# Kernel tuning notes

Hardware: AMD Instinct MI355X
Metric: run time of the kernel (lower is better)

Reference implementation:

```python
import jax, jax.numpy as jnp
import numpy as np

N, E, D_IN, HID, HEADS, D_OUT, R = 20000, 640000, 256, 128, 4, 128, 32
NEG_SLOPE = 0.2  # PyG GATConv default


def setup_inputs() -> dict:
    key = jax.random.key(0)
    ks = jax.random.split(key, 12)
    s = 0.05
    return {
        "x": jax.random.normal(ks[0], (N, D_IN), jnp.float32),
        "edge_index": jax.random.randint(ks[1], (2, E), 0, N, dtype=jnp.int64),
        "edge_type": jax.random.randint(ks[2], (E,), 0, R, dtype=jnp.int64),
        "rel_emb": jax.random.normal(ks[3], (R, D_IN), jnp.float32) * s,
        "W1": jax.random.normal(ks[4], (D_IN, HEADS * HID), jnp.float32) * s,
        "att_src1": jax.random.normal(ks[5], (HEADS, HID), jnp.float32) * s,
        "att_dst1": jax.random.normal(ks[6], (HEADS, HID), jnp.float32) * s,
        "b1": jnp.zeros((HEADS * HID,), jnp.float32),
        "W2": jax.random.normal(ks[7], (HEADS * HID, D_OUT), jnp.float32) * s,
        "att_src2": jax.random.normal(ks[8], (1, D_OUT), jnp.float32) * s,
        "att_dst2": jax.random.normal(ks[9], (1, D_OUT), jnp.float32) * s,
        "b2": jnp.zeros((D_OUT,), jnp.float32),
    }


def _gat_conv(x, src, dst, W, a_src, a_dst, bias, heads, ch):
    """PyG GATConv (eval mode, self loops already in src/dst)."""
    n = x.shape[0]
    h = (x @ W).reshape(n, heads, ch)                      # [N,H,C]
    alpha_s = jnp.einsum('nhc,hc->nh', h, a_src)           # [N,H]
    alpha_d = jnp.einsum('nhc,hc->nh', h, a_dst)
    e = jax.nn.leaky_relu(alpha_s[src] + alpha_d[dst], NEG_SLOPE)  # [E,H]
    # segment softmax over incoming edges of each dst node
    m = jax.ops.segment_max(e, dst, num_segments=n)        # [N,H]
    p = jnp.exp(e - m[dst])
    denom = jax.ops.segment_sum(p, dst, num_segments=n)
    alpha = p / (denom[dst] + 1e-16)                       # [E,H]
    out = jax.ops.segment_sum(h[src] * alpha[:, :, None], dst, num_segments=n)
    return out.reshape(n, heads * ch) + bias


def reference(x, edge_index, edge_type, rel_emb, W1, att_src1, att_dst1, b1,
              W2, att_src2, att_dst2, b2):
    src, dst = edge_index[0], edge_index[1]
    # relational feature injection: x_mod[src] += rel_emb[edge_type]
    x_mod = x.at[src].add(rel_emb[edge_type])
    # GATConv adds self loops by default
    loop = jnp.arange(N, dtype=src.dtype)
    s2 = jnp.concatenate([src, loop])
    d2 = jnp.concatenate([dst, loop])
    h = _gat_conv(x_mod, s2, d2, W1, att_src1, att_dst1, b1, HEADS, HID)
    h = jax.nn.elu(h)
    return _gat_conv(h, s2, d2, W2, att_src2, att_dst2, b2, 1, D_OUT)
```

## Files before the change

kernel.cpp:

```cpp
#include <hip/hip_runtime.h>


#define D_IN   256
#define HID1   512
#define NHEADS 4
#define CH1    128
#define DOUT   128
#define NREL   32
#define NEG_SLOPE 0.2f
#define M_PAD  20096

static __device__ __forceinline__ float b2f(unsigned short u) {
  union { unsigned int i; float f; } v; v.i = ((unsigned int)u) << 16; return v.f;
}
static __device__ __forceinline__ unsigned short f2b(float f) {
  union { float f; unsigned int i; } v; v.f = f;
  unsigned int x = v.i;
  return (unsigned short)((x + 0x7fffu + ((x >> 16) & 1u)) >> 16);
}
static __device__ __forceinline__ float lrelu(float x) {
  return x > 0.f ? x : NEG_SLOPE * x;
}
static __device__ __forceinline__ void acc8(float* acc, float w, uint4 r) {
  unsigned int u;
  union { unsigned int i; float f; } cl, ch;
  u = r.x; cl.i = u << 16; ch.i = u & 0xffff0000u; acc[0] += w * cl.f; acc[1] += w * ch.f;
  u = r.y; cl.i = u << 16; ch.i = u & 0xffff0000u; acc[2] += w * cl.f; acc[3] += w * ch.f;
  u = r.z; cl.i = u << 16; ch.i = u & 0xffff0000u; acc[4] += w * cl.f; acc[5] += w * ch.f;
  u = r.w; cl.i = u << 16; ch.i = u & 0xffff0000u; acc[6] += w * cl.f; acc[7] += w * ch.f;
}

typedef __attribute__((ext_vector_type(8))) short bf16x8;
typedef __attribute__((ext_vector_type(4))) float f32x4;

__global__ void prep_kernel(const int* __restrict__ src, const int* __restrict__ dst,
                            const int* __restrict__ et, int* __restrict__ counts,
                            int* __restrict__ deg, int E, int eb,
                            const float* __restrict__ W1, const float* __restrict__ W2,
                            unsigned short* __restrict__ W1T, unsigned short* __restrict__ W2T) {
  int b = blockIdx.x;
  if (b < eb) {
    int e = b * 256 + threadIdx.x;
    if (e >= E) return;
    atomicAdd(&counts[(size_t)src[e] * NREL + et[e]], 1);
    atomicAdd(&deg[dst[e]], 1);
  } else {
    int idx = (b - eb) * 256 + threadIdx.x;
    if (idx < D_IN * HID1) {
      int r = idx / HID1, c = idx % HID1;
      W1T[(size_t)c * D_IN + r] = f2b(W1[idx]);
    } else {
      int k = idx - D_IN * HID1;
      if (k < HID1 * DOUT) {
        int r = k / DOUT, c = k % DOUT;
        W2T[(size_t)c * HID1 + r] = f2b(W2[k]);
      }
    }
  }
}

__global__ void scan_local(const int* __restrict__ in, int* __restrict__ out,
                           int* __restrict__ bsum, int n) {
  __shared__ int wsum[4];
  int t = threadIdx.x;
  int base = blockIdx.x * 1024 + t * 4;
  int v0 = (base + 0 < n) ? in[base + 0] : 0;
  int v1 = (base + 1 < n) ? in[base + 1] : 0;
  int v2 = (base + 2 < n) ? in[base + 2] : 0;
  int v3 = (base + 3 < n) ? in[base + 3] : 0;
  int s = v0 + v1 + v2 + v3;
  int lane = t & 63, w = t >> 6;
  int sc = s;
  for (int off = 1; off < 64; off <<= 1) {
    int u = __shfl_up(sc, off);
    if (lane >= off) sc += u;
  }
  if (lane == 63) wsum[w] = sc;
  __syncthreads();
  int woff = 0;
  for (int i = 0; i < w; ++i) woff += wsum[i];
  int excl = woff + sc - s;
  if (base + 0 < n) out[base + 0] = excl;
  if (base + 1 < n) out[base + 1] = excl + v0;
  if (base + 2 < n) out[base + 2] = excl + v0 + v1;
  if (base + 3 < n) out[base + 3] = excl + v0 + v1 + v2;
  if (t == 255) bsum[blockIdx.x] = woff + sc;
}

__global__ void scan_blocks(int* __restrict__ bsum, int nb,
                            int* __restrict__ offsets, int n) {
  int t = threadIdx.x;
  int v = (t < nb) ? bsum[t] : 0;
  int sc = v;
  for (int off = 1; off < 64; off <<= 1) {
    int u = __shfl_up(sc, off);
    if (t >= off) sc += u;
  }
  if (t < nb) bsum[t] = sc - v;
  if (t == nb - 1) offsets[n] = v;
}

__global__ void scatter_kernel(const int* __restrict__ src, const int* __restrict__ dst,
                               const int* __restrict__ offsets, const int* __restrict__ bsum,
                               int* __restrict__ cursor, int* __restrict__ csr_src, int E) {
  int e = blockIdx.x * 256 + threadIdx.x;
  if (e >= E) return;
  int d = dst[e];
  int pos = offsets[d] + bsum[d >> 10] + atomicAdd(&cursor[d], 1);
  csr_src[pos] = src[e];
}

__global__ void xmod_kernel(const float* __restrict__ x,
                            const int* __restrict__ counts,
                            const float* __restrict__ rel,
                            unsigned short* __restrict__ x_modb, int n_nodes) {
  __shared__ int cnt[NREL];
  int node = blockIdx.x;
  if (threadIdx.x < NREL) cnt[threadIdx.x] = counts[(size_t)node * NREL + threadIdx.x];
  __syncthreads();
  int k = threadIdx.x;
  float v = x[(size_t)node * D_IN + k];
  for (int r = 0; r < NREL; ++r) {
    int c = cnt[r];
    if (c) v += (float)c * rel[r * D_IN + k];
  }
  x_modb[(size_t)node * D_IN + k] = f2b(v);
}

template <int BM, int NH>
__global__ __launch_bounds__(256) void mfma_gemm(
    const unsigned short* __restrict__ A, const unsigned short* __restrict__ BT,
    unsigned short* __restrict__ C, int M, int N, int K,
    const float* __restrict__ att_s, const float* __restrict__ att_d,
    float* __restrict__ as_out, float* __restrict__ ad_out) {
  constexpr int MFR = BM / 32;
  __shared__ __align__(16) unsigned short Asl[BM * 32];
  __shared__ __align__(16) unsigned short Bsl[128 * 32];
  int tid = threadIdx.x;
  int m0 = blockIdx.y * BM, n0 = blockIdx.x * 128;
  int lane = tid & 63, wv = tid >> 6;
  int wm = wv & 1, wn = wv >> 1;
  int l16 = lane & 15, quad = lane >> 4;
  int lr = lane >> 2, lseg = lane & 3;

  f32x4 acc[MFR][4];
#pragma unroll
  for (int i = 0; i < MFR; ++i)
#pragma unroll
    for (int j = 0; j < 4; ++j) acc[i][j] = (f32x4)(0.f);

  for (int k0 = 0; k0 < K; k0 += 32) {
#pragma unroll
    for (int c = wv; c < BM / 16; c += 4) {
      int gr = m0 + c * 16 + lr; gr = gr < M ? gr : M - 1;
      __builtin_amdgcn_global_load_lds(
          (const __attribute__((address_space(1))) void*)(A + (size_t)gr * K + k0 + lseg * 8),
          (__attribute__((address_space(3))) void*)(&Asl[c * 512]), 16, 0, 0);
    }
#pragma unroll
    for (int c = wv; c < 8; c += 4) {
      int gr = n0 + c * 16 + lr;
      __builtin_amdgcn_global_load_lds(
          (const __attribute__((address_space(1))) void*)(BT + (size_t)gr * K + k0 + lseg * 8),
          (__attribute__((address_space(3))) void*)(&Bsl[c * 512]), 16, 0, 0);
    }
    __syncthreads();
    bf16x8 af[MFR], bfr[4];
#pragma unroll
    for (int mf = 0; mf < MFR; ++mf)
      af[mf] = *(const bf16x8*)(&Asl[(wm * (BM / 2) + mf * 16 + l16) * 32 + quad * 8]);
#pragma unroll
    for (int nf = 0; nf < 4; ++nf)
      bfr[nf] = *(const bf16x8*)(&Bsl[(wn * 64 + nf * 16 + l16) * 32 + quad * 8]);
#pragma unroll
    for (int mf = 0; mf < MFR; ++mf)
#pragma unroll
      for (int nf = 0; nf < 4; ++nf)
        acc[mf][nf] = __builtin_amdgcn_mfma_f32_16x16x32_bf16(af[mf], bfr[nf], acc[mf][nf], 0, 0, 0);
    __syncthreads();
  }
#pragma unroll
  for (int mf = 0; mf < MFR; ++mf)
#pragma unroll
    for (int nf = 0; nf < 4; ++nf)
#pragma unroll
      for (int r = 0; r < 4; ++r) {
        int row = m0 + wm * (BM / 2) + mf * 16 + quad * 4 + r;
        int col = n0 + wn * 64 + nf * 16 + l16;
        C[(size_t)row * N + col] = f2b(acc[mf][nf][r]);
      }
  int head = blockIdx.x;
  float asw[4], adw[4];
#pragma unroll
  for (int nf = 0; nf < 4; ++nf) {
    int cl = wn * 64 + nf * 16 + l16;
    asw[nf] = att_s[head * 128 + cl];
    adw[nf] = att_d[head * 128 + cl];
  }
#pragma unroll
  for (int mf = 0; mf < MFR; ++mf)
#pragma unroll
    for (int r = 0; r < 4; ++r) {
      float sd = acc[mf][0][r] * asw[0] + acc[mf][1][r] * asw[1] +
                 acc[mf][2][r] * asw[2] + acc[mf][3][r] * asw[3];
      float dd = acc[mf][0][r] * adw[0] + acc[mf][1][r] * adw[1] +
                 acc[mf][2][r] * adw[2] + acc[mf][3][r] * adw[3];
#pragma unroll
      for (int off = 1; off < 16; off <<= 1) {
        sd += __shfl_xor(sd, off);
        dd += __shfl_xor(dd, off);
      }
      int row = m0 + wm * (BM / 2) + mf * 16 + quad * 4 + r;
      if (l16 == 0 && row < M) {
        atomicAdd(&as_out[row * NH + head], sd);
        atomicAdd(&ad_out[row * NH + head], dd);
      }
    }
}

__global__ __launch_bounds__(256) void aggregate1_kernel(
    const unsigned short* __restrict__ h1b,
    const float* __restrict__ as1, const float* __restrict__ ad1,
    const int* __restrict__ offsets, const int* __restrict__ bsum,
    const int* __restrict__ csr_src,
    const float* __restrict__ bias, unsigned short* __restrict__ h2b, int n_nodes) {
  int node = blockIdx.x * 4 + (threadIdx.x >> 6);
  if (node >= n_nodes) return;
  int lane = threadIdx.x & 63;
  int g = lane >> 5, l32 = lane & 31;
  int head = l32 >> 3;
  int lo = offsets[node] + bsum[node >> 10];
  int hi = offsets[node + 1] + bsum[(node + 1) >> 10];
  float4 asn = ((const float4*)as1)[node];
  float4 ad4 = ((const float4*)ad1)[node];
  float ad_own = head == 0 ? ad4.x : head == 1 ? ad4.y : head == 2 ? ad4.z : ad4.w;
  float as_own = head == 0 ? asn.x : head == 1 ? asn.y : head == 2 ? asn.z : asn.w;

  const uint4* h1v = (const uint4*)h1b;
  float acc[16];
#pragma unroll
  for (int k = 0; k < 16; ++k) acc[k] = 0.f;
  float denom = 0.f;

  int nit = (hi - lo + 1) >> 1;
  int j = lo + g;
  bool valid = j < hi;
  int s = valid ? csr_src[j] : node;
  float asv = as1[s * 4 + head];
  for (int i = 0; i < nit; ++i) {
    int jn = j + 2;
    bool vn = jn < hi;
    int sn = vn ? csr_src[jn] : node;
    float asv_n = as1[sn * 4 + head];
    uint4 h0 = h1v[(size_t)s * 64 + l32 * 2];
    uint4 h1r = h1v[(size_t)s * 64 + l32 * 2 + 1];
    float w = valid ? __expf(lrelu(asv + ad_own)) : 0.f;
    acc8(acc, w, h0); acc8(acc + 8, w, h1r);
    denom += w;
    j = jn; valid = vn; s = sn; asv = asv_n;
  }
  if (g == 0) {
    uint4 h0 = h1v[(size_t)node * 64 + l32 * 2];
    uint4 h1r = h1v[(size_t)node * 64 + l32 * 2 + 1];
    float w = __expf(lrelu(as_own + ad_own));
    acc8(acc, w, h0); acc8(acc + 8, w, h1r);
    denom += w;
  }
#pragma unroll
  for (int k = 0; k < 16; ++k) acc[k] += __shfl_xor(acc[k], 32);
  denom += __shfl_xor(denom, 32);
  if (g == 0) {
    float inv = 1.f / (denom + 1e-16f);
    unsigned int od[8];
#pragma unroll
    for (int q = 0; q < 8; ++q) {
      float vlo = acc[2 * q] * inv + bias[l32 * 16 + 2 * q];
      float vhi = acc[2 * q + 1] * inv + bias[l32 * 16 + 2 * q + 1];
      vlo = vlo > 0.f ? vlo : expm1f(vlo);
      vhi = vhi > 0.f ? vhi : expm1f(vhi);
      od[q] = (unsigned int)f2b(vlo) | ((unsigned int)f2b(vhi) << 16);
    }
    uint4 o0; o0.x = od[0]; o0.y = od[1]; o0.z = od[2]; o0.w = od[3];
    uint4 o1; o1.x = od[4]; o1.y = od[5]; o1.z = od[6]; o1.w = od[7];
    ((uint4*)h2b)[(size_t)node * 64 + l32 * 2] = o0;
    ((uint4*)h2b)[(size_t)node * 64 + l32 * 2 + 1] = o1;
  }
}

__global__ __launch_bounds__(256) void aggregate2_kernel(
    const unsigned short* __restrict__ t2b,
    const float* __restrict__ as2, const float* __restrict__ ad2,
    const int* __restrict__ offsets, const int* __restrict__ bsum,
    const int* __restrict__ csr_src,
    const float* __restrict__ bias, float* __restrict__ out, int n_nodes) {
  int node = blockIdx.x * 4 + (threadIdx.x >> 6);
  if (node >= n_nodes) return;
  int lane = threadIdx.x & 63;
  int g = lane >> 4, l16 = lane & 15;
  int lo = offsets[node] + bsum[node >> 10];
  int hi = offsets[node + 1] + bsum[(node + 1) >> 10];
  float ad = ad2[node];

  const uint4* t2v = (const uint4*)t2b;
  float acc[8] = {0.f, 0.f, 0.f, 0.f, 0.f, 0.f, 0.f, 0.f};
  float denom = 0.f;
  int nit = (hi - lo + 3) >> 2;
  int j = lo + g;
  bool valid = j < hi;
  int s = valid ? csr_src[j] : node;
  float asv = as2[s];
  for (int i = 0; i < nit; ++i) {
    int jn = j + 4;
    bool vn = jn < hi;
    int sn = vn ? csr_src[jn] : node;
    float asv_n = as2[sn];
    uint4 tv = t2v[(size_t)s * 16 + l16];
    float w = valid ? __expf(lrelu(asv + ad)) : 0.f;
    acc8(acc, w, tv);
    denom += w;
    j = jn; valid = vn; s = sn; asv = asv_n;
  }
  if (g == 0) {
    uint4 tv = t2v[(size_t)node * 16 + l16];
    float w = __expf(lrelu(as2[node] + ad));
    acc8(acc, w, tv);
    denom += w;
  }
#pragma unroll
  for (int k = 0; k < 8; ++k) {
    acc[k] += __shfl_xor(acc[k], 16);
    acc[k] += __shfl_xor(acc[k], 32);
  }
  denom += __shfl_xor(denom, 16);
  denom += __shfl_xor(denom, 32);
  if (g == 0) {
    float inv = 1.f / (denom + 1e-16f);
    float4 o0, o1;
    o0.x = acc[0] * inv + bias[l16 * 8 + 0];
    o0.y = acc[1] * inv + bias[l16 * 8 + 1];
    o0.z = acc[2] * inv + bias[l16 * 8 + 2];
    o0.w = acc[3] * inv + bias[l16 * 8 + 3];
    o1.x = acc[4] * inv + bias[l16 * 8 + 4];
    o1.y = acc[5] * inv + bias[l16 * 8 + 5];
    o1.z = acc[6] * inv + bias[l16 * 8 + 6];
    o1.w = acc[7] * inv + bias[l16 * 8 + 7];
    *(float4*)(out + (size_t)node * DOUT + l16 * 8) = o0;
    *(float4*)(out + (size_t)node * DOUT + l16 * 8 + 4) = o1;
  }
}

extern "C" void kernel_launch(void* const* d_in, const int* in_sizes, int n_in,
                              void* d_out, int out_size, void* d_ws, size_t ws_size,
                              hipStream_t stream) {
  const float* x     = (const float*)d_in[0];
  const int* ei      = (const int*)d_in[1];
  const int* etype   = (const int*)d_in[2];
  const float* rel   = (const float*)d_in[3];
  const float* W1    = (const float*)d_in[4];
  const float* at_s1 = (const float*)d_in[5];
  const float* at_d1 = (const float*)d_in[6];
  const float* b1    = (const float*)d_in[7];
  const float* W2    = (const float*)d_in[8];
  const float* at_s2 = (const float*)d_in[9];
  const float* at_d2 = (const float*)d_in[10];
  const float* b2v   = (const float*)d_in[11];
  float* out         = (float*)d_out;

  const int N = in_sizes[0] / D_IN;
  const int E = in_sizes[2];
  const int* srcv = ei;
  const int* dstv = ei + E;

  char* p = (char*)d_ws;
  auto carve = [&](size_t bytes) -> char* {
    char* r = p; p += (bytes + 255) & ~(size_t)255; return r;
  };
  int*   counts  = (int*)carve((size_t)N * NREL * 4);
  int*   deg     = (int*)carve((size_t)N * 4);
  int*   offsets = (int*)carve(((size_t)N + 1) * 4);
  int*   cursor  = (int*)carve((size_t)N * 4);
  int*   bsum    = (int*)carve(64 * 4);
  float* as1     = (float*)carve((size_t)N * NHEADS * 4);
  float* ad1     = (float*)carve((size_t)N * NHEADS * 4);
  float* as2     = (float*)carve((size_t)N * 4);
  float* ad2     = (float*)carve((size_t)N * 4);
  size_t zero_bytes = (size_t)(p - (char*)counts);
  int*   csr_src = (int*)carve((size_t)E * 4);
  unsigned short* W1T    = (unsigned short*)carve((size_t)HID1 * D_IN * 2);
  unsigned short* W2T    = (unsigned short*)carve((size_t)DOUT * HID1 * 2);
  unsigned short* x_modb = (unsigned short*)carve((size_t)M_PAD * D_IN * 2);
  unsigned short* h1b    = (unsigned short*)carve((size_t)M_PAD * HID1 * 2);
  unsigned short* h2b    = (unsigned short*)carve((size_t)M_PAD * HID1 * 2);
  unsigned short* t2b    = (unsigned short*)carve((size_t)M_PAD * DOUT * 2);

  hipMemsetAsync(counts, 0, zero_bytes, stream);

  int eb = (E + 255) / 256;
  int cb = (D_IN * HID1 + HID1 * DOUT + 255) / 256;
  int nb = (N + 1023) / 1024;
  prep_kernel<<<eb + cb, 256, 0, stream>>>(srcv, dstv, etype, counts, deg, E, eb,
                                           W1, W2, W1T, W2T);
  scan_local<<<nb, 256, 0, stream>>>(deg, offsets, bsum, N);
  scan_blocks<<<1, 64, 0, stream>>>(bsum, nb, offsets, N);
  scatter_kernel<<<eb, 256, 0, stream>>>(srcv, dstv, offsets, bsum, cursor, csr_src, E);
  xmod_kernel<<<N, 256, 0, stream>>>(x, counts, rel, x_modb, N);
  mfma_gemm<128, NHEADS><<<dim3(HID1 / 128, M_PAD / 128), 256, 0, stream>>>(
      x_modb, W1T, h1b, N, HID1, D_IN, at_s1, at_d1, as1, ad1);
  aggregate1_kernel<<<(N + 3) / 4, 256, 0, stream>>>(h1b, as1, ad1, offsets, bsum,
                                                     csr_src, b1, h2b, N);
  mfma_gemm<64, 1><<<dim3(DOUT / 128, M_PAD / 64), 256, 0, stream>>>(
      h2b, W2T, t2b, N, DOUT, HID1, at_s2, at_d2, as2, ad2);
  aggregate2_kernel<<<(N + 3) / 4, 256, 0, stream>>>(t2b, as2, ad2, offsets, bsum,
                                                     csr_src, b2v, out, N);
}
```

Baseline: 382.0 us.

## Precompute edge weights, stage neighbor rows via LDS loads, fold layer-2 attention into aggregate1

The change adds separate kernels that compute the per-edge softmax numerators (exp of leaky-relu) over the CSR order, which requires building a csr_dst array. The aggregation kernels now gather neighbor feature rows in batches straight into shared memory with global_load_lds, one full wave per node. The layer-2 attention projections are computed algebraically as h2·(W2·att) inside aggregate1, using vectors precomputed in scan_blocks, so the second GEMM no longer needs its atomic alpha epilogue. The xmod kernel is also vectorized to four nodes per block with float4 loads. In exchange it adds two edge-sized kernels, extra workspace traffic for the weights and csr_dst, and explicit waitcnt barriers that serialize each batch's loads.

```diff
diff --git a/kernel.cpp b/kernel.cpp
--- a/kernel.cpp
+++ b/kernel.cpp
@@ -4,15 +4,16 @@
 #define D_IN   256
 #define HID1   512
 #define NHEADS 4
-#define CH1    128
 #define DOUT   128
 #define NREL   32
 #define NEG_SLOPE 0.2f
 #define M_PAD  20096
-
-static __device__ __forceinline__ float b2f(unsigned short u) {
-  union { unsigned int i; float f; } v; v.i = ((unsigned int)u) << 16; return v.f;
-}
+#define DB1    8
+#define DB2    16
+
+#define WAIT_VM0()   __builtin_amdgcn_s_waitcnt(0x0f70)
+#define WAIT_LGKM0() __builtin_amdgcn_s_waitcnt(0xc07f)
+
 static __device__ __forceinline__ unsigned short f2b(float f) {
   union { float f; unsigned int i; } v; v.f = f;
   unsigned int x = v.i;
@@ -88,46 +89,72 @@
 }
 
 __global__ void scan_blocks(int* __restrict__ bsum, int nb,
-                            int* __restrict__ offsets, int n) {
+                            int* __restrict__ offsets, int n,
+                            const float* __restrict__ W2,
+                            const float* __restrict__ att_s2, const float* __restrict__ att_d2,
+                            float* __restrict__ vs, float* __restrict__ vd) {
   int t = threadIdx.x;
-  int v = (t < nb) ? bsum[t] : 0;
-  int sc = v;
-  for (int off = 1; off < 64; off <<= 1) {
-    int u = __shfl_up(sc, off);
-    if (t >= off) sc += u;
-  }
-  if (t < nb) bsum[t] = sc - v;
-  if (t == nb - 1) offsets[n] = v;
+  if (t < 64) {
+    int v = (t < nb) ? bsum[t] : 0;
+    int sc = v;
+    for (int off = 1; off < 64; off <<= 1) {
+      int u = __shfl_up(sc, off);
+      if (t >= off) sc += u;
+    }
+    if (t < nb) bsum[t] = sc - v;
+    if (t == nb - 1) offsets[n] = v;
+  }
+#pragma unroll
+  for (int rr = 0; rr < 2; ++rr) {
+    int r = t * 2 + rr;
+    float ss = 0.f, dd = 0.f;
+    for (int c = 0; c < DOUT; ++c) {
+      float wv = W2[(size_t)r * DOUT + c];
+      ss += wv * att_s2[c];
+      dd += wv * att_d2[c];
+    }
+    vs[r] = ss; vd[r] = dd;
+  }
 }
 
 __global__ void scatter_kernel(const int* __restrict__ src, const int* __restrict__ dst,
                                const int* __restrict__ offsets, const int* __restrict__ bsum,
-                               int* __restrict__ cursor, int* __restrict__ csr_src, int E) {
+                               int* __restrict__ cursor, int* __restrict__ csr_src,
+                               int* __restrict__ csr_dst, int E) {
   int e = blockIdx.x * 256 + threadIdx.x;
   if (e >= E) return;
   int d = dst[e];
   int pos = offsets[d] + bsum[d >> 10] + atomicAdd(&cursor[d], 1);
   csr_src[pos] = src[e];
-}
-
-__global__ void xmod_kernel(const float* __restrict__ x,
-                            const int* __restrict__ counts,
-                            const float* __restrict__ rel,
-                            unsigned short* __restrict__ x_modb, int n_nodes) {
-  __shared__ int cnt[NREL];
-  int node = blockIdx.x;
-  if (threadIdx.x < NREL) cnt[threadIdx.x] = counts[(size_t)node * NREL + threadIdx.x];
-  __syncthreads();
-  int k = threadIdx.x;
-  float v = x[(size_t)node * D_IN + k];
+  csr_dst[pos] = d;
+}
+
+__global__ __launch_bounds__(256) void xmod_kernel(
+    const float* __restrict__ x, const int* __restrict__ counts,
+    const float* __restrict__ rel, unsigned short* __restrict__ x_modb, int n_nodes) {
+  int wv = threadIdx.x >> 6;
+  int node = blockIdx.x * 4 + wv;
+  if (node >= n_nodes) return;
+  int l = threadIdx.x & 63;
+  int cnt_l = counts[(size_t)node * NREL + (l & 31)];
+  const float4* x4 = (const float4*)x;
+  const float4* rel4 = (const float4*)rel;
+  float4 v = x4[(size_t)node * 64 + l];
+#pragma unroll
   for (int r = 0; r < NREL; ++r) {
-    int c = cnt[r];
-    if (c) v += (float)c * rel[r * D_IN + k];
-  }
-  x_modb[(size_t)node * D_IN + k] = f2b(v);
-}
-
-template <int BM, int NH>
+    int c = __shfl(cnt_l, r);
+    if (c) {
+      float4 rv = rel4[r * 64 + l];
+      float fc = (float)c;
+      v.x += fc * rv.x; v.y += fc * rv.y; v.z += fc * rv.z; v.w += fc * rv.w;
+    }
+  }
+  ushort4 o;
+  o.x = f2b(v.x); o.y = f2b(v.y); o.z = f2b(v.z); o.w = f2b(v.w);
+  *(ushort4*)(x_modb + (size_t)node * D_IN + l * 4) = o;
+}
+
+template <int BM, bool ALPHA>
 __global__ __launch_bounds__(256) void mfma_gemm(
     const unsigned short* __restrict__ A, const unsigned short* __restrict__ BT,
     unsigned short* __restrict__ C, int M, int N, int K,
@@ -189,164 +216,183 @@
         int col = n0 + wn * 64 + nf * 16 + l16;
         C[(size_t)row * N + col] = f2b(acc[mf][nf][r]);
       }
-  int head = blockIdx.x;
-  float asw[4], adw[4];
-#pragma unroll
-  for (int nf = 0; nf < 4; ++nf) {
-    int cl = wn * 64 + nf * 16 + l16;
-    asw[nf] = att_s[head * 128 + cl];
-    adw[nf] = att_d[head * 128 + cl];
-  }
-#pragma unroll
-  for (int mf = 0; mf < MFR; ++mf)
-#pragma unroll
-    for (int r = 0; r < 4; ++r) {
-      float sd = acc[mf][0][r] * asw[0] + acc[mf][1][r] * asw[1] +
-                 acc[mf][2][r] * asw[2] + acc[mf][3][r] * asw[3];
-      float dd = acc[mf][0][r] * adw[0] + acc[mf][1][r] * adw[1] +
-                 acc[mf][2][r] * adw[2] + acc[mf][3][r] * adw[3];
-#pragma unroll
-      for (int off = 1; off < 16; off <<= 1) {
-        sd += __shfl_xor(sd, off);
-        dd += __shfl_xor(dd, off);
+  if constexpr (ALPHA) {
+    int head = blockIdx.x;
+    float asw[4], adw[4];
+#pragma unroll
+    for (int nf = 0; nf < 4; ++nf) {
+      int cl = wn * 64 + nf * 16 + l16;
+      asw[nf] = att_s[head * 128 + cl];
+      adw[nf] = att_d[head * 128 + cl];
+    }
+#pragma unroll
+    for (int mf = 0; mf < MFR; ++mf)
+#pragma unroll
+      for (int r = 0; r < 4; ++r) {
+        float sd = acc[mf][0][r] * asw[0] + acc[mf][1][r] * asw[1] +
+                   acc[mf][2][r] * asw[2] + acc[mf][3][r] * asw[3];
+        float dd = acc[mf][0][r] * adw[0] + acc[mf][1][r] * adw[1] +
+                   acc[mf][2][r] * adw[2] + acc[mf][3][r] * adw[3];
+#pragma unroll
+        for (int off = 1; off < 16; off <<= 1) {
+          sd += __shfl_xor(sd, off);
+          dd += __shfl_xor(dd, off);
+        }
+        int row = m0 + wm * (BM / 2) + mf * 16 + quad * 4 + r;
+        if (l16 == 0 && row < M) {
+          atomicAdd(&as_out[row * NHEADS + head], sd);
+          atomicAdd(&ad_out[row * NHEADS + head], dd);
+        }
       }
-      int row = m0 + wm * (BM / 2) + mf * 16 + quad * 4 + r;
-      if (l16 == 0 && row < M) {
-        atomicAdd(&as_out[row * NH + head], sd);
-        atomicAdd(&ad_out[row * NH + head], dd);
-      }
-    }
+  }
+}
+
+__global__ void weights1_kernel(const int* __restrict__ csr_src, const int* __restrict__ csr_dst,
+                                const float* __restrict__ as1, const float* __restrict__ ad1,
+                                float* __restrict__ wls, int E) {
+  int e = blockIdx.x * 256 + threadIdx.x;
+  if (e >= E) return;
+  float4 a = ((const float4*)as1)[csr_src[e]];
+  float4 b = ((const float4*)ad1)[csr_dst[e]];
+  float4 w;
+  w.x = __expf(lrelu(a.x + b.x));
+  w.y = __expf(lrelu(a.y + b.y));
+  w.z = __expf(lrelu(a.z + b.z));
+  w.w = __expf(lrelu(a.w + b.w));
+  ((float4*)wls)[e] = w;
+}
+
+__global__ void weights2_kernel(const int* __restrict__ csr_src, const int* __restrict__ csr_dst,
+                                const float* __restrict__ as2, const float* __restrict__ ad2,
+                                float* __restrict__ w2, int E) {
+  int e = blockIdx.x * 256 + threadIdx.x;
+  if (e >= E) return;
+  w2[e] = __expf(lrelu(as2[csr_src[e]] + ad2[csr_dst[e]]));
 }
 
 __global__ __launch_bounds__(256) void aggregate1_kernel(
     const unsigned short* __restrict__ h1b,
     const float* __restrict__ as1, const float* __restrict__ ad1,
     const int* __restrict__ offsets, const int* __restrict__ bsum,
-    const int* __restrict__ csr_src,
-    const float* __restrict__ bias, unsigned short* __restrict__ h2b, int n_nodes) {
-  int node = blockIdx.x * 4 + (threadIdx.x >> 6);
+    const int* __restrict__ csr_src, const float* __restrict__ wls,
+    const float* __restrict__ bias, const float* __restrict__ vs,
+    const float* __restrict__ vd, unsigned short* __restrict__ h2b,
+    float* __restrict__ as2, float* __restrict__ ad2, int n_nodes) {
+  __shared__ __align__(16) unsigned short ring[4][DB1 * 512];
+  int wv = threadIdx.x >> 6;
+  int node = blockIdx.x * 4 + wv;
   if (node >= n_nodes) return;
   int lane = threadIdx.x & 63;
-  int g = lane >> 5, l32 = lane & 31;
-  int head = l32 >> 3;
+  int head = lane >> 4;
   int lo = offsets[node] + bsum[node >> 10];
   int hi = offsets[node + 1] + bsum[(node + 1) >> 10];
+  unsigned short* myring = ring[wv];
+  float acc[8] = {0.f, 0.f, 0.f, 0.f, 0.f, 0.f, 0.f, 0.f};
+  float denom = 0.f;
+
+  for (int j = lo; j < hi; j += DB1) {
+    int nb = hi - j; nb = nb < DB1 ? nb : DB1;
+    int sidx = j + (lane & 7); sidx = sidx < hi ? sidx : hi - 1;
+    int sv = csr_src[sidx];
+    float wl = wls[(size_t)sidx * 4 + head];
+    for (int k = 0; k < nb; ++k) {
+      int s = __shfl(sv, k);
+      __builtin_amdgcn_global_load_lds(
+          (const __attribute__((address_space(1))) void*)(h1b + (size_t)s * HID1 + lane * 8),
+          (__attribute__((address_space(3))) void*)(&myring[k * 512]), 16, 0, 0);
+    }
+    WAIT_VM0();
+    for (int k = 0; k < nb; ++k) {
+      float w = __shfl(wl, (head << 4) | k);
+      uint4 r = *(const uint4*)(&myring[k * 512 + lane * 8]);
+      acc8(acc, w, r);
+      denom += w;
+    }
+    WAIT_LGKM0();
+  }
   float4 asn = ((const float4*)as1)[node];
   float4 ad4 = ((const float4*)ad1)[node];
+  float as_own = head == 0 ? asn.x : head == 1 ? asn.y : head == 2 ? asn.z : asn.w;
   float ad_own = head == 0 ? ad4.x : head == 1 ? ad4.y : head == 2 ? ad4.z : ad4.w;
-  float as_own = head == 0 ? asn.x : head == 1 ? asn.y : head == 2 ? asn.z : asn.w;
-
-  const uint4* h1v = (const uint4*)h1b;
-  float acc[16];
-#pragma unroll
-  for (int k = 0; k < 16; ++k) acc[k] = 0.f;
-  float denom = 0.f;
-
-  int nit = (hi - lo + 1) >> 1;
-  int j = lo + g;
-  bool valid = j < hi;
-  int s = valid ? csr_src[j] : node;
-  float asv = as1[s * 4 + head];
-  for (int i = 0; i < nit; ++i) {
-    int jn = j + 2;
-    bool vn = jn < hi;
-    int sn = vn ? csr_src[jn] : node;
-    float asv_n = as1[sn * 4 + head];
-    uint4 h0 = h1v[(size_t)s * 64 + l32 * 2];
-    uint4 h1r = h1v[(size_t)s * 64 + l32 * 2 + 1];
-    float w = valid ? __expf(lrelu(asv + ad_own)) : 0.f;
-    acc8(acc, w, h0); acc8(acc + 8, w, h1r);
-    denom += w;
-    j = jn; valid = vn; s = sn; asv = asv_n;
-  }
-  if (g == 0) {
-    uint4 h0 = h1v[(size_t)node * 64 + l32 * 2];
-    uint4 h1r = h1v[(size_t)node * 64 + l32 * 2 + 1];
-    float w = __expf(lrelu(as_own + ad_own));
-    acc8(acc, w, h0); acc8(acc + 8, w, h1r);
-    denom += w;
-  }
-#pragma unroll
-  for (int k = 0; k < 16; ++k) acc[k] += __shfl_xor(acc[k], 32);
-  denom += __shfl_xor(denom, 32);
-  if (g == 0) {
-    float inv = 1.f / (denom + 1e-16f);
-    unsigned int od[8];
-#pragma unroll
-    for (int q = 0; q < 8; ++q) {
-      float vlo = acc[2 * q] * inv + bias[l32 * 16 + 2 * q];
-      float vhi = acc[2 * q + 1] * inv + bias[l32 * 16 + 2 * q + 1];
-      vlo = vlo > 0.f ? vlo : expm1f(vlo);
-      vhi = vhi > 0.f ? vhi : expm1f(vhi);
-      od[q] = (unsigned int)f2b(vlo) | ((unsigned int)f2b(vhi) << 16);
-    }
-    uint4 o0; o0.x = od[0]; o0.y = od[1]; o0.z = od[2]; o0.w = od[3];
-    uint4 o1; o1.x = od[4]; o1.y = od[5]; o1.z = od[6]; o1.w = od[7];
-    ((uint4*)h2b)[(size_t)node * 64 + l32 * 2] = o0;
-    ((uint4*)h2b)[(size_t)node * 64 + l32 * 2 + 1] = o1;
-  }
+  float wself = __expf(lrelu(as_own + ad_own));
+  uint4 own = *(const uint4*)(h1b + (size_t)node * HID1 + lane * 8);
+  acc8(acc, wself, own);
+  denom += wself;
+
+  float inv = 1.f / (denom + 1e-16f);
+  float ss = 0.f, dd = 0.f;
+  unsigned int od[4];
+#pragma unroll
+  for (int q = 0; q < 4; ++q) {
+    int ch = lane * 8 + 2 * q;
+    float vlo = acc[2 * q] * inv + bias[ch];
+    float vhi = acc[2 * q + 1] * inv + bias[ch + 1];
+    vlo = vlo > 0.f ? vlo : expm1f(vlo);
+    vhi = vhi > 0.f ? vhi : expm1f(vhi);
+    ss += vlo * vs[ch] + vhi * vs[ch + 1];
+    dd += vlo * vd[ch] + vhi * vd[ch + 1];
+    od[q] = (unsigned int)f2b(vlo) | ((unsigned int)f2b(vhi) << 16);
+  }
+  uint4 o; o.x = od[0]; o.y = od[1]; o.z = od[2]; o.w = od[3];
+  *(uint4*)(h2b + (size_t)node * HID1 + lane * 8) = o;
+  for (int off = 32; off; off >>= 1) {
+    ss += __shfl_xor(ss, off);
+    dd += __shfl_xor(dd, off);
+  }
+  if (lane == 0) { as2[node] = ss; ad2[node] = dd; }
 }
 
 __global__ __launch_bounds__(256) void aggregate2_kernel(
     const unsigned short* __restrict__ t2b,
     const float* __restrict__ as2, const float* __restrict__ ad2,
     const int* __restrict__ offsets, const int* __restrict__ bsum,
-    const int* __restrict__ csr_src,
+    const int* __restrict__ csr_src, const float* __restrict__ w2,
     const float* __restrict__ bias, float* __restrict__ out, int n_nodes) {
-  int node = blockIdx.x * 4 + (threadIdx.x >> 6);
+  __shared__ __align__(16) unsigned short ring[4][DB2 * 128];
+  int wv = threadIdx.x >> 6;
+  int node = blockIdx.x * 4 + wv;
   if (node >= n_nodes) return;
   int lane = threadIdx.x & 63;
-  int g = lane >> 4, l16 = lane & 15;
   int lo = offsets[node] + bsum[node >> 10];
   int hi = offsets[node + 1] + bsum[(node + 1) >> 10];
-  float ad = ad2[node];
-
-  const uint4* t2v = (const uint4*)t2b;
-  float acc[8] = {0.f, 0.f, 0.f, 0.f, 0.f, 0.f, 0.f, 0.f};
-  float denom = 0.f;
-  int nit = (hi - lo + 3) >> 2;
-  int j = lo + g;
-  bool valid = j < hi;
-  int s = valid ? csr_src[j] : node;
-  float asv = as2[s];
-  for (int i = 0; i < nit; ++i) {
-    int jn = j + 4;
-    bool vn = jn < hi;
-    int sn = vn ? csr_src[jn] : node;
-    float asv_n = as2[sn];
-    uint4 tv = t2v[(size_t)s * 16 + l16];
-    float w = valid ? __expf(lrelu(asv + ad)) : 0.f;
-    acc8(acc, w, tv);
-    denom += w;
-    j = jn; valid = vn; s = sn; asv = asv_n;
-  }
-  if (g == 0) {
-    uint4 tv = t2v[(size_t)node * 16 + l16];
-    float w = __expf(lrelu(as2[node] + ad));
-    acc8(acc, w, tv);
-    denom += w;
-  }
-#pragma unroll
-  for (int k = 0; k < 8; ++k) {
-    acc[k] += __shfl_xor(acc[k], 16);
-    acc[k] += __shfl_xor(acc[k], 32);
-  }
-  denom += __shfl_xor(denom, 16);
-  denom += __shfl_xor(denom, 32);
-  if (g == 0) {
-    float inv = 1.f / (denom + 1e-16f);
-    float4 o0, o1;
-    o0.x = acc[0] * inv + bias[l16 * 8 + 0];
-    o0.y = acc[1] * inv + bias[l16 * 8 + 1];
-    o0.z = acc[2] * inv + bias[l16 * 8 + 2];
-    o0.w = acc[3] * inv + bias[l16 * 8 + 3];
-    o1.x = acc[4] * inv + bias[l16 * 8 + 4];
-    o1.y = acc[5] * inv + bias[l16 * 8 + 5];
-    o1.z = acc[6] * inv + bias[l16 * 8 + 6];
-    o1.w = acc[7] * inv + bias[l16 * 8 + 7];
-    *(float4*)(out + (size_t)node * DOUT + l16 * 8) = o0;
-    *(float4*)(out + (size_t)node * DOUT + l16 * 8 + 4) = o1;
-  }
+  unsigned short* myring = ring[wv];
+  float a0 = 0.f, a1 = 0.f, denom = 0.f;
+
+  for (int j = lo; j < hi; j += DB2) {
+    int nb = hi - j; nb = nb < DB2 ? nb : DB2;
+    int sidx = j + (lane & 15); sidx = sidx < hi ? sidx : hi - 1;
+    int sv = csr_src[sidx];
+    float wl = w2[sidx];
+    for (int k = 0; k < nb; ++k) {
+      int s = __shfl(sv, k);
+      __builtin_amdgcn_global_load_lds(
+          (const __attribute__((address_space(1))) void*)(t2b + (size_t)s * DOUT + lane * 2),
+          (__attribute__((address_space(3))) void*)(&myring[k * 128]), 4, 0, 0);
+    }
+    WAIT_VM0();
+    for (int k = 0; k < nb; ++k) {
+      float w = __shfl(wl, k);
+      unsigned int u = *(const unsigned int*)(&myring[k * 128 + lane * 2]);
+      union { unsigned int i; float f; } cl, ch;
+      cl.i = u << 16; ch.i = u & 0xffff0000u;
+      a0 += w * cl.f; a1 += w * ch.f;
+      denom += w;
+    }
+    WAIT_LGKM0();
+  }
+  float wself = __expf(lrelu(as2[node] + ad2[node]));
+  {
+    unsigned int u = *(const unsigned int*)(t2b + (size_t)node * DOUT + lane * 2);
+    union { unsigned int i; float f; } cl, ch;
+    cl.i = u << 16; ch.i = u & 0xffff0000u;
+    a0 += wself * cl.f; a1 += wself * ch.f;
+    denom += wself;
+  }
+  float inv = 1.f / (denom + 1e-16f);
+  float2 o;
+  o.x = a0 * inv + bias[lane * 2];
+  o.y = a1 * inv + bias[lane * 2 + 1];
+  *(float2*)(out + (size_t)node * DOUT + lane * 2) = o;
 }
 
 extern "C" void kernel_launch(void* const* d_in, const int* in_sizes, int n_in,
@@ -382,10 +428,15 @@
   int*   bsum    = (int*)carve(64 * 4);
   float* as1     = (float*)carve((size_t)N * NHEADS * 4);
   float* ad1     = (float*)carve((size_t)N * NHEADS * 4);
+  size_t zero_bytes = (size_t)(p - (char*)counts);
   float* as2     = (float*)carve((size_t)N * 4);
   float* ad2     = (float*)carve((size_t)N * 4);
-  size_t zero_bytes = (size_t)(p - (char*)counts);
+  float* vs      = (float*)carve((size_t)HID1 * 4);
+  float* vd      = (float*)carve((size_t)HID1 * 4);
   int*   csr_src = (int*)carve((size_t)E * 4);
+  int*   csr_dst = (int*)carve((size_t)E * 4);
+  float* wls     = (float*)carve((size_t)E * NHEADS * 4);
+  float* w2      = (float*)carve((size_t)E * 4);
   unsigned short* W1T    = (unsigned short*)carve((size_t)HID1 * D_IN * 2);
   unsigned short* W2T    = (unsigned short*)carve((size_t)DOUT * HID1 * 2);
   unsigned short* x_modb = (unsigned short*)carve((size_t)M_PAD * D_IN * 2);
@@ -401,15 +452,18 @@
   prep_kernel<<<eb + cb, 256, 0, stream>>>(srcv, dstv, etype, counts, deg, E, eb,
                                            W1, W2, W1T, W2T);
   scan_local<<<nb, 256, 0, stream>>>(deg, offsets, bsum, N);
-  scan_blocks<<<1, 64, 0, stream>>>(bsum, nb, offsets, N);
-  scatter_kernel<<<eb, 256, 0, stream>>>(srcv, dstv, offsets, bsum, cursor, csr_src, E);
-  xmod_kernel<<<N, 256, 0, stream>>>(x, counts, rel, x_modb, N);
-  mfma_gemm<128, NHEADS><<<dim3(HID1 / 128, M_PAD / 128), 256, 0, stream>>>(
+  scan_blocks<<<1, 256, 0, stream>>>(bsum, nb, offsets, N, W2, at_s2, at_d2, vs, vd);
+  scatter_kernel<<<eb, 256, 0, stream>>>(srcv, dstv, offsets, bsum, cursor,
+                                         csr_src, csr_dst, E);
+  xmod_kernel<<<(N + 3) / 4, 256, 0, stream>>>(x, counts, rel, x_modb, N);
+  mfma_gemm<128, true><<<dim3(HID1 / 128, M_PAD / 128), 256, 0, stream>>>(
       x_modb, W1T, h1b, N, HID1, D_IN, at_s1, at_d1, as1, ad1);
-  aggregate1_kernel<<<(N + 3) / 4, 256, 0, stream>>>(h1b, as1, ad1, offsets, bsum,
-                                                     csr_src, b1, h2b, N);
-  mfma_gemm<64, 1><<<dim3(DOUT / 128, M_PAD / 64), 256, 0, stream>>>(
-      h2b, W2T, t2b, N, DOUT, HID1, at_s2, at_d2, as2, ad2);
-  aggregate2_kernel<<<(N + 3) / 4, 256, 0, stream>>>(t2b, as2, ad2, offsets, bsum,
-                                                     csr_src, b2v, out, N);
-}
+  weights1_kernel<<<eb, 256, 0, stream>>>(csr_src, csr_dst, as1, ad1, wls, E);
+  aggregate1_kernel<<<(N + 3) / 4, 256, 0, stream>>>(
+      h1b, as1, ad1, offsets, bsum, csr_src, wls, b1, vs, vd, h2b, as2, ad2, N);
+  weights2_kernel<<<eb, 256, 0, stream>>>(csr_src, csr_dst, as2, ad2, w2, E);
+  mfma_gemm<64, false><<<dim3(DOUT / 128, M_PAD / 64), 256, 0, stream>>>(
+      h2b, W2T, t2b, N, DOUT, HID1, nullptr, nullptr, nullptr, nullptr);
+  aggregate2_kernel<<<(N + 3) / 4, 256, 0, stream>>>(
+      t2b, as2, ad2, offsets, bsum, csr_src, w2, b2v, out, N);
+}
```

Result: slower. 404.7 us (+5.9%).

## Precompute edge attention weights in scatter, fold layer-2 alpha into aggregate1

Applied to the files above, without the earlier changes.

Several changes at once. The CSR scatter now runs after the first GEMM and writes per-edge exp(leaky_relu) weights for all four heads, so aggregate1 no longer gathers source alphas or computes exp per edge. Layer-2 alpha_src/alpha_dst are obtained by folding W2 with the attention vectors (computed in the scan kernel) and dotted with the ELU output inside aggregate1, which removes the atomic alpha epilogue from the second GEMM. xmod is rewritten to one wave per node with float4 loads. The cost is an extra E×4 float weight buffer that must be written and read back, and some loss of overlap because the scatter now waits on the first GEMM.

```diff
diff --git a/kernel.cpp b/kernel.cpp
--- a/kernel.cpp
+++ b/kernel.cpp
@@ -4,15 +4,11 @@
 #define D_IN   256
 #define HID1   512
 #define NHEADS 4
-#define CH1    128
 #define DOUT   128
 #define NREL   32
 #define NEG_SLOPE 0.2f
 #define M_PAD  20096
 
-static __device__ __forceinline__ float b2f(unsigned short u) {
-  union { unsigned int i; float f; } v; v.i = ((unsigned int)u) << 16; return v.f;
-}
 static __device__ __forceinline__ unsigned short f2b(float f) {
   union { float f; unsigned int i; } v; v.f = f;
   unsigned int x = v.i;
@@ -88,46 +84,81 @@
 }
 
 __global__ void scan_blocks(int* __restrict__ bsum, int nb,
-                            int* __restrict__ offsets, int n) {
+                            int* __restrict__ offsets, int n,
+                            const float* __restrict__ W2,
+                            const float* __restrict__ att_s2, const float* __restrict__ att_d2,
+                            float* __restrict__ vs, float* __restrict__ vd) {
   int t = threadIdx.x;
-  int v = (t < nb) ? bsum[t] : 0;
-  int sc = v;
-  for (int off = 1; off < 64; off <<= 1) {
-    int u = __shfl_up(sc, off);
-    if (t >= off) sc += u;
-  }
-  if (t < nb) bsum[t] = sc - v;
-  if (t == nb - 1) offsets[n] = v;
-}
-
-__global__ void scatter_kernel(const int* __restrict__ src, const int* __restrict__ dst,
-                               const int* __restrict__ offsets, const int* __restrict__ bsum,
-                               int* __restrict__ cursor, int* __restrict__ csr_src, int E) {
+  if (t < 64) {
+    int v = (t < nb) ? bsum[t] : 0;
+    int sc = v;
+    for (int off = 1; off < 64; off <<= 1) {
+      int u = __shfl_up(sc, off);
+      if (t >= off) sc += u;
+    }
+    if (t < nb) bsum[t] = sc - v;
+    if (t == nb - 1) offsets[n] = v;
+  }
+#pragma unroll
+  for (int rr = 0; rr < 2; ++rr) {
+    int r = t * 2 + rr;
+    float ss = 0.f, dd = 0.f;
+    for (int c = 0; c < DOUT; ++c) {
+      float wv = W2[(size_t)r * DOUT + c];
+      ss += wv * att_s2[c];
+      dd += wv * att_d2[c];
+    }
+    vs[r] = ss; vd[r] = dd;
+  }
+}
+
+__global__ void scatter_w_kernel(const int* __restrict__ src, const int* __restrict__ dst,
+                                 const int* __restrict__ offsets, const int* __restrict__ bsum,
+                                 int* __restrict__ cursor, int* __restrict__ csr_src,
+                                 const float* __restrict__ as1, const float* __restrict__ ad1,
+                                 float* __restrict__ wls, int E) {
   int e = blockIdx.x * 256 + threadIdx.x;
   if (e >= E) return;
   int d = dst[e];
+  int s = src[e];
   int pos = offsets[d] + bsum[d >> 10] + atomicAdd(&cursor[d], 1);
-  csr_src[pos] = src[e];
-}
-
-__global__ void xmod_kernel(const float* __restrict__ x,
-                            const int* __restrict__ counts,
-                            const float* __restrict__ rel,
-                            unsigned short* __restrict__ x_modb, int n_nodes) {
-  __shared__ int cnt[NREL];
-  int node = blockIdx.x;
-  if (threadIdx.x < NREL) cnt[threadIdx.x] = counts[(size_t)node * NREL + threadIdx.x];
-  __syncthreads();
-  int k = threadIdx.x;
-  float v = x[(size_t)node * D_IN + k];
+  csr_src[pos] = s;
+  float4 a = ((const float4*)as1)[s];
+  float4 b = ((const float4*)ad1)[d];
+  float4 w;
+  w.x = __expf(lrelu(a.x + b.x));
+  w.y = __expf(lrelu(a.y + b.y));
+  w.z = __expf(lrelu(a.z + b.z));
+  w.w = __expf(lrelu(a.w + b.w));
+  ((float4*)wls)[pos] = w;
+}
+
+__global__ __launch_bounds__(256) void xmod_kernel(
+    const float* __restrict__ x, const int* __restrict__ counts,
+    const float* __restrict__ rel, unsigned short* __restrict__ x_modb, int n_nodes) {
+  int wv = threadIdx.x >> 6;
+  int node = blockIdx.x * 4 + wv;
+  if (node >= n_nodes) return;
+  int l = threadIdx.x & 63;
+  int cnt_l = counts[(size_t)node * NREL + (l & 31)];
+  const float4* x4 = (const float4*)x;
+  const float4* rel4 = (const float4*)rel;
+  float4 v = x4[(size_t)node * 64 + l];
+#pragma unroll
   for (int r = 0; r < NREL; ++r) {
-    int c = cnt[r];
-    if (c) v += (float)c * rel[r * D_IN + k];
-  }
-  x_modb[(size_t)node * D_IN + k] = f2b(v);
-}
-
-template <int BM, int NH>
+    int c = __shfl(cnt_l, r);
+    if (c) {
+      float4 rv = rel4[r * 64 + l];
+      float fc = (float)c;
+      v.x += fc * rv.x; v.y += fc * rv.y; v.z += fc * rv.z; v.w += fc * rv.w;
+    }
+  }
+  ushort4 o;
+  o.x = f2b(v.x); o.y = f2b(v.y); o.z = f2b(v.z); o.w = f2b(v.w);
+  *(ushort4*)(x_modb + (size_t)node * D_IN + l * 4) = o;
+}
+
+template <int BM, bool ALPHA>
 __global__ __launch_bounds__(256) void mfma_gemm(
     const unsigned short* __restrict__ A, const unsigned short* __restrict__ BT,
     unsigned short* __restrict__ C, int M, int N, int K,
@@ -189,41 +220,45 @@
         int col = n0 + wn * 64 + nf * 16 + l16;
         C[(size_t)row * N + col] = f2b(acc[mf][nf][r]);
       }
-  int head = blockIdx.x;
-  float asw[4], adw[4];
-#pragma unroll
-  for (int nf = 0; nf < 4; ++nf) {
-    int cl = wn * 64 + nf * 16 + l16;
-    asw[nf] = att_s[head * 128 + cl];
-    adw[nf] = att_d[head * 128 + cl];
-  }
-#pragma unroll
-  for (int mf = 0; mf < MFR; ++mf)
-#pragma unroll
-    for (int r = 0; r < 4; ++r) {
-      float sd = acc[mf][0][r] * asw[0] + acc[mf][1][r] * asw[1] +
-                 acc[mf][2][r] * asw[2] + acc[mf][3][r] * asw[3];
-      float dd = acc[mf][0][r] * adw[0] + acc[mf][1][r] * adw[1] +
-                 acc[mf][2][r] * adw[2] + acc[mf][3][r] * adw[3];
-#pragma unroll
-      for (int off = 1; off < 16; off <<= 1) {
-        sd += __shfl_xor(sd, off);
-        dd += __shfl_xor(dd, off);
+  if constexpr (ALPHA) {
+    int head = blockIdx.x;
+    float asw[4], adw[4];
+#pragma unroll
+    for (int nf = 0; nf < 4; ++nf) {
+      int cl = wn * 64 + nf * 16 + l16;
+      asw[nf] = att_s[head * 128 + cl];
+      adw[nf] = att_d[head * 128 + cl];
+    }
+#pragma unroll
+    for (int mf = 0; mf < MFR; ++mf)
+#pragma unroll
+      for (int r = 0; r < 4; ++r) {
+        float sd = acc[mf][0][r] * asw[0] + acc[mf][1][r] * asw[1] +
+                   acc[mf][2][r] * asw[2] + acc[mf][3][r] * asw[3];
+        float dd = acc[mf][0][r] * adw[0] + acc[mf][1][r] * adw[1] +
+                   acc[mf][2][r] * adw[2] + acc[mf][3][r] * adw[3];
+#pragma unroll
+        for (int off = 1; off < 16; off <<= 1) {
+          sd += __shfl_xor(sd, off);
+          dd += __shfl_xor(dd, off);
+        }
+        int row = m0 + wm * (BM / 2) + mf * 16 + quad * 4 + r;
+        if (l16 == 0 && row < M) {
+          atomicAdd(&as_out[row * NHEADS + head], sd);
+          atomicAdd(&ad_out[row * NHEADS + head], dd);
+        }
       }
-      int row = m0 + wm * (BM / 2) + mf * 16 + quad * 4 + r;
-      if (l16 == 0 && row < M) {
-        atomicAdd(&as_out[row * NH + head], sd);
-        atomicAdd(&ad_out[row * NH + head], dd);
-      }
-    }
+  }
 }
 
 __global__ __launch_bounds__(256) void aggregate1_kernel(
     const unsigned short* __restrict__ h1b,
     const float* __restrict__ as1, const float* __restrict__ ad1,
     const int* __restrict__ offsets, const int* __restrict__ bsum,
-    const int* __restrict__ csr_src,
-    const float* __restrict__ bias, unsigned short* __restrict__ h2b, int n_nodes) {
+    const int* __restrict__ csr_src, const float* __restrict__ wls,
+    const float* __restrict__ bias, const float* __restrict__ vs,
+    const float* __restrict__ vd, unsigned short* __restrict__ h2b,
+    float* __restrict__ as2, float* __restrict__ ad2, int n_nodes) {
   int node = blockIdx.x * 4 + (threadIdx.x >> 6);
   if (node >= n_nodes) return;
   int lane = threadIdx.x & 63;
@@ -231,10 +266,6 @@
   int head = l32 >> 3;
   int lo = offsets[node] + bsum[node >> 10];
   int hi = offsets[node + 1] + bsum[(node + 1) >> 10];
-  float4 asn = ((const float4*)as1)[node];
-  float4 ad4 = ((const float4*)ad1)[node];
-  float ad_own = head == 0 ? ad4.x : head == 1 ? ad4.y : head == 2 ? ad4.z : ad4.w;
-  float as_own = head == 0 ? asn.x : head == 1 ? asn.y : head == 2 ? asn.z : asn.w;
 
   const uint4* h1v = (const uint4*)h1b;
   float acc[16];
@@ -246,44 +277,57 @@
   int j = lo + g;
   bool valid = j < hi;
   int s = valid ? csr_src[j] : node;
-  float asv = as1[s * 4 + head];
+  float wc = valid ? wls[(size_t)j * 4 + head] : 0.f;
   for (int i = 0; i < nit; ++i) {
     int jn = j + 2;
     bool vn = jn < hi;
     int sn = vn ? csr_src[jn] : node;
-    float asv_n = as1[sn * 4 + head];
+    float wn = vn ? wls[(size_t)jn * 4 + head] : 0.f;
     uint4 h0 = h1v[(size_t)s * 64 + l32 * 2];
     uint4 h1r = h1v[(size_t)s * 64 + l32 * 2 + 1];
-    float w = valid ? __expf(lrelu(asv + ad_own)) : 0.f;
-    acc8(acc, w, h0); acc8(acc + 8, w, h1r);
-    denom += w;
-    j = jn; valid = vn; s = sn; asv = asv_n;
-  }
+    acc8(acc, wc, h0); acc8(acc + 8, wc, h1r);
+    denom += wc;
+    j = jn; valid = vn; s = sn; wc = wn;
+  }
+  float4 asn = ((const float4*)as1)[node];
+  float4 ad4 = ((const float4*)ad1)[node];
+  float as_own = head == 0 ? asn.x : head == 1 ? asn.y : head == 2 ? asn.z : asn.w;
+  float ad_own = head == 0 ? ad4.x : head == 1 ? ad4.y : head == 2 ? ad4.z : ad4.w;
   if (g == 0) {
+    float wself = __expf(lrelu(as_own + ad_own));
     uint4 h0 = h1v[(size_t)node * 64 + l32 * 2];
     uint4 h1r = h1v[(size_t)node * 64 + l32 * 2 + 1];
-    float w = __expf(lrelu(as_own + ad_own));
-    acc8(acc, w, h0); acc8(acc + 8, w, h1r);
-    denom += w;
+    acc8(acc, wself, h0); acc8(acc + 8, wself, h1r);
+    denom += wself;
   }
 #pragma unroll
   for (int k = 0; k < 16; ++k) acc[k] += __shfl_xor(acc[k], 32);
   denom += __shfl_xor(denom, 32);
   if (g == 0) {
     float inv = 1.f / (denom + 1e-16f);
+    float ss = 0.f, dd = 0.f;
     unsigned int od[8];
 #pragma unroll
     for (int q = 0; q < 8; ++q) {
-      float vlo = acc[2 * q] * inv + bias[l32 * 16 + 2 * q];
-      float vhi = acc[2 * q + 1] * inv + bias[l32 * 16 + 2 * q + 1];
+      int ch = l32 * 16 + 2 * q;
+      float vlo = acc[2 * q] * inv + bias[ch];
+      float vhi = acc[2 * q + 1] * inv + bias[ch + 1];
       vlo = vlo > 0.f ? vlo : expm1f(vlo);
       vhi = vhi > 0.f ? vhi : expm1f(vhi);
+      ss += vlo * vs[ch] + vhi * vs[ch + 1];
+      dd += vlo * vd[ch] + vhi * vd[ch + 1];
       od[q] = (unsigned int)f2b(vlo) | ((unsigned int)f2b(vhi) << 16);
     }
     uint4 o0; o0.x = od[0]; o0.y = od[1]; o0.z = od[2]; o0.w = od[3];
     uint4 o1; o1.x = od[4]; o1.y = od[5]; o1.z = od[6]; o1.w = od[7];
     ((uint4*)h2b)[(size_t)node * 64 + l32 * 2] = o0;
     ((uint4*)h2b)[(size_t)node * 64 + l32 * 2 + 1] = o1;
+#pragma unroll
+    for (int off = 16; off; off >>= 1) {
+      ss += __shfl_xor(ss, off);
+      dd += __shfl_xor(dd, off);
+    }
+    if (l32 == 0) { as2[node] = ss; ad2[node] = dd; }
   }
 }
 
@@ -382,10 +426,13 @@
   int*   bsum    = (int*)carve(64 * 4);
   float* as1     = (float*)carve((size_t)N * NHEADS * 4);
   float* ad1     = (float*)carve((size_t)N * NHEADS * 4);
+  size_t zero_bytes = (size_t)(p - (char*)counts);
   float* as2     = (float*)carve((size_t)N * 4);
   float* ad2     = (float*)carve((size_t)N * 4);
-  size_t zero_bytes = (size_t)(p - (char*)counts);
+  float* vs      = (float*)carve((size_t)HID1 * 4);
+  float* vd      = (float*)carve((size_t)HID1 * 4);
   int*   csr_src = (int*)carve((size_t)E * 4);
+  float* wls     = (float*)carve((size_t)E * NHEADS * 4);
   unsigned short* W1T    = (unsigned short*)carve((size_t)HID1 * D_IN * 2);
   unsigned short* W2T    = (unsigned short*)carve((size_t)DOUT * HID1 * 2);
   unsigned short* x_modb = (unsigned short*)carve((size_t)M_PAD * D_IN * 2);
@@ -401,15 +448,16 @@
   prep_kernel<<<eb + cb, 256, 0, stream>>>(srcv, dstv, etype, counts, deg, E, eb,
                                            W1, W2, W1T, W2T);
   scan_local<<<nb, 256, 0, stream>>>(deg, offsets, bsum, N);
-  scan_blocks<<<1, 64, 0, stream>>>(bsum, nb, offsets, N);
-  scatter_kernel<<<eb, 256, 0, stream>>>(srcv, dstv, offsets, bsum, cursor, csr_src, E);
-  xmod_kernel<<<N, 256, 0, stream>>>(x, counts, rel, x_modb, N);
-  mfma_gemm<128, NHEADS><<<dim3(HID1 / 128, M_PAD / 128), 256, 0, stream>>>(
+  scan_blocks<<<1, 256, 0, stream>>>(bsum, nb, offsets, N, W2, at_s2, at_d2, vs, vd);
+  xmod_kernel<<<(N + 3) / 4, 256, 0, stream>>>(x, counts, rel, x_modb, N);
+  mfma_gemm<128, true><<<dim3(HID1 / 128, M_PAD / 128), 256, 0, stream>>>(
       x_modb, W1T, h1b, N, HID1, D_IN, at_s1, at_d1, as1, ad1);
-  aggregate1_kernel<<<(N + 3) / 4, 256, 0, stream>>>(h1b, as1, ad1, offsets, bsum,
-                                                     csr_src, b1, h2b, N);
-  mfma_gemm<64, 1><<<dim3(DOUT / 128, M_PAD / 64), 256, 0, stream>>>(
-      h2b, W2T, t2b, N, DOUT, HID1, at_s2, at_d2, as2, ad2);
-  aggregate2_kernel<<<(N + 3) / 4, 256, 0, stream>>>(t2b, as2, ad2, offsets, bsum,
-                                                     csr_src, b2v, out, N);
-}
+  scatter_w_kernel<<<eb, 256, 0, stream>>>(srcv, dstv, offsets, bsum, cursor,
+                                           csr_src, as1, ad1, wls, E);
+  aggregate1_kernel<<<(N + 3) / 4, 256, 0, stream>>>(
+      h1b, as1, ad1, offsets, bsum, csr_src, wls, b1, vs, vd, h2b, as2, ad2, N);
+  mfma_gemm<64, false><<<dim3(DOUT / 128, M_PAD / 64), 256, 0, stream>>>(
+      h2b, W2T, t2b, N, DOUT, HID1, nullptr, nullptr, nullptr, nullptr);
+  aggregate2_kernel<<<(N + 3) / 4, 256, 0, stream>>>(
+      t2b, as2, ad2, offsets, bsum, csr_src, b2v, out, N);
+}
```

Result: no change. 384.5 us (+0.6%).
